# Optimization experiments

Hardware: AMD Instinct MI355X
Metric: run time of the kernel (lower is better)

Reference implementation:

```python
import jax, jax.numpy as jnp
import numpy as np
import math

GROUPS = 32
EPS = 1e-5
N_HEADS = 8  # channels=512 / num_head_channels=64


def group_norm(x, w, b):
    # x: [B, C, T]; GroupNorm over (channels-in-group, T)
    B, C, T = x.shape
    xg = x.reshape(B, GROUPS, C // GROUPS * T)
    mu = xg.mean(axis=-1, keepdims=True)
    var = xg.var(axis=-1, keepdims=True)
    xn = ((xg - mu) * jax.lax.rsqrt(var + EPS)).reshape(B, C, T)
    return xn * w[None, :, None] + b[None, :, None]


def setup_inputs() -> dict:
    key = jax.random.key(0)
    ks = jax.random.split(key, 7)
    C = 512
    return {
        "x": jax.random.normal(ks[0], (8, C, 32, 32), dtype=jnp.float32),
        "norm_w": jax.random.normal(ks[1], (C,), dtype=jnp.float32),
        "norm_b": jax.random.normal(ks[2], (C,), dtype=jnp.float32),
        "qkv_w": jax.random.normal(ks[3], (3 * C, C), dtype=jnp.float32) * 0.02,
        "qkv_b": jax.random.normal(ks[4], (3 * C,), dtype=jnp.float32) * 0.02,
        "proj_w": jax.random.normal(ks[5], (C, C), dtype=jnp.float32) * 0.02,
        "proj_b": jax.random.normal(ks[6], (C,), dtype=jnp.float32) * 0.02,
    }


def reference(x, norm_w, norm_b, qkv_w, qkv_b, proj_w, proj_b):
    b, c, H, W = x.shape
    T = H * W
    xf = x.reshape(b, c, T)
    xn = group_norm(xf, norm_w, norm_b)
    # 1x1 conv1d == channel matmul: [3C, C] x [B, C, T] -> [B, 3C, T]
    qkv = jnp.einsum('oc,bct->bot', qkv_w, xn) + qkv_b[None, :, None]
    ch = c // N_HEADS
    qkv = qkv.reshape(b * N_HEADS, 3 * ch, T)
    q, k, v = qkv[:, :ch], qkv[:, ch:2 * ch], qkv[:, 2 * ch:]
    scale = 1.0 / math.sqrt(math.sqrt(ch))
    # [BH, T, T] score matrix (explicit, as in the original)
    weight = jnp.einsum('bct,bcs->bts', q * scale, k * scale)
    weight = jax.nn.softmax(weight.astype(jnp.float32), axis=-1).astype(qkv.dtype)
    a = jnp.einsum('bts,bcs->bct', weight, v).reshape(b, c, T)
    hout = jnp.einsum('oc,bct->bot', proj_w, a) + proj_b[None, :, None]
    return (xf + hout).reshape(b, c, H, W)
```

## Files before the change

### kernel.cpp

```cpp
#include <hip/hip_runtime.h>
#include <math.h>

typedef float f32x4_t __attribute__((ext_vector_type(4)));
typedef short bf16x8_t __attribute__((ext_vector_type(8)));

#define B_   8
#define C_   512
#define T_   1024
#define NH_  8
#define CH_  64
#define EPSF 1e-5f

#define MFMA16(a, b, c) __builtin_amdgcn_mfma_f32_16x16x32_bf16((a), (b), (c), 0, 0, 0)

#define GLD16(gp, lp) __builtin_amdgcn_global_load_lds( \
    (const __attribute__((address_space(1))) unsigned int*)(gp), \
    (__attribute__((address_space(3))) unsigned int*)(lp), 16, 0, 0)

__device__ __forceinline__ unsigned short f2bf(float f) {
  union { float f; unsigned u; } v; v.f = f;
  unsigned r = v.u + 0x7FFFu + ((v.u >> 16) & 1u);
  return (unsigned short)(r >> 16);
}

__global__ __launch_bounds__(256) void prep_gn_kernel(
    const float* __restrict__ x, const float* __restrict__ w,
    const float* __restrict__ bvec, unsigned short* __restrict__ xnT,
    const float* __restrict__ qw_f, const float* __restrict__ pw_f,
    unsigned short* __restrict__ qw, unsigned short* __restrict__ pw)
{
  int tid = threadIdx.x;
  if (blockIdx.x >= 256) {
    int idx = (blockIdx.x - 256) * 256 + tid;
    const int N1 = 1536 * 512 / 4;
    const int N2 = 512 * 512 / 4;
    if (idx < N1) {
      float4 v = ((const float4*)qw_f)[idx];
      uint2 o;
      o.x = (unsigned)f2bf(v.x) | ((unsigned)f2bf(v.y) << 16);
      o.y = (unsigned)f2bf(v.z) | ((unsigned)f2bf(v.w) << 16);
      ((uint2*)qw)[idx] = o;
    } else if (idx < N1 + N2) {
      int j = idx - N1;
      float4 v = ((const float4*)pw_f)[j];
      uint2 o;
      o.x = (unsigned)f2bf(v.x) | ((unsigned)f2bf(v.y) << 16);
      o.y = (unsigned)f2bf(v.z) | ((unsigned)f2bf(v.w) << 16);
      ((uint2*)pw)[j] = o;
    }
    return;
  }

  int blk = blockIdx.x;
  int b = blk >> 5, g = blk & 31;
  const float* xp = x + ((size_t)(b * C_ + g * 16)) * T_;
  const int N = 16 * T_;

  float s = 0.f, s2 = 0.f;
  for (int i = tid * 4; i < N; i += 256 * 4) {
    float4 v = *(const float4*)(xp + i);
    s  += v.x + v.y + v.z + v.w;
    s2 += v.x * v.x + v.y * v.y + v.z * v.z + v.w * v.w;
  }
  for (int off = 32; off; off >>= 1) {
    s  += __shfl_down(s,  off, 64);
    s2 += __shfl_down(s2, off, 64);
  }
  __shared__ float rs_[4], r2_[4];
  __shared__ float mu_s, rsig_s;
  int wid = tid >> 6, lane = tid & 63;
  if (lane == 0) { rs_[wid] = s; r2_[wid] = s2; }
  __syncthreads();
  if (tid == 0) {
    float ts = rs_[0] + rs_[1] + rs_[2] + rs_[3];
    float t2 = r2_[0] + r2_[1] + r2_[2] + r2_[3];
    float mu = ts / (float)N;
    float var = t2 / (float)N - mu * mu;
    mu_s = mu;
    rsig_s = rsqrtf(var + EPSF);
  }
  __syncthreads();
  float mu = mu_s, rs = rsig_s;

  float wl[16], bl[16];
  for (int c = 0; c < 16; ++c) { wl[c] = w[g * 16 + c]; bl[c] = bvec[g * 16 + c]; }

  for (int t = tid; t < T_; t += 256) {
    unsigned short buf[16] __attribute__((aligned(16)));
    for (int c = 0; c < 16; ++c) {
      float val = xp[(size_t)c * T_ + t];
      buf[c] = f2bf((val - mu) * rs * wl[c] + bl[c]);
    }
    unsigned short* dst = xnT + ((size_t)b * T_ + t) * C_ + g * 16;
    *(uint4*)dst       = *(uint4*)buf;
    *(uint4*)(dst + 8) = *(uint4*)(buf + 8);
  }
}

__global__ __launch_bounds__(256) void gemm_qkv_kernel(
    const unsigned short* __restrict__ W, const unsigned short* __restrict__ xnT,
    const float* __restrict__ bias,
    unsigned short* __restrict__ q_t, unsigned short* __restrict__ k_t,
    unsigned short* __restrict__ v_c)
{
  int b = blockIdx.z;
  int m0 = blockIdx.y * 128, n0 = blockIdx.x * 128;
  int tid = threadIdx.x;
  int w = tid >> 6, lane = tid & 63, quad = lane >> 4, lr = lane & 15;
  int wm = w >> 1, wn = w & 1;

  __shared__ __align__(16) unsigned short Asl[2][128][32];
  __shared__ __align__(16) unsigned short Bsl[2][128][32];

  f32x4_t acc[4][4];
  for (int i = 0; i < 4; ++i)
    for (int j = 0; j < 4; ++j) acc[i][j] = (f32x4_t){0.f, 0.f, 0.f, 0.f};

  int ur = tid >> 2, uk = (tid & 3) * 8;
  const unsigned short* Ap = W + (size_t)(m0 + ur) * C_ + uk;
  const unsigned short* Bp = xnT + ((size_t)b * T_ + n0 + ur) * C_ + uk;

#define STAGE_QKV(buf, k0)                                        \
  do {                                                            \
    GLD16(Ap + (k0),            &Asl[buf][w * 16][0]);            \
    GLD16(Ap + 64 * C_ + (k0),  &Asl[buf][64 + w * 16][0]);       \
    GLD16(Bp + (k0),            &Bsl[buf][w * 16][0]);            \
    GLD16(Bp + 64 * C_ + (k0),  &Bsl[buf][64 + w * 16][0]);       \
  } while (0)

  STAGE_QKV(0, 0);
  __syncthreads();

  int cur = 0;
  for (int k0 = 0; k0 < C_; k0 += 32) {
    if (k0 + 32 < C_) STAGE_QKV(cur ^ 1, k0 + 32);
    bf16x8_t af[4], bfv[4];
    for (int i = 0; i < 4; ++i) af[i]  = *(bf16x8_t*)&Asl[cur][wm * 64 + i * 16 + lr][quad * 8];
    for (int j = 0; j < 4; ++j) bfv[j] = *(bf16x8_t*)&Bsl[cur][wn * 64 + j * 16 + lr][quad * 8];
    for (int i = 0; i < 4; ++i)
      for (int j = 0; j < 4; ++j)
        acc[i][j] = MFMA16(af[i], bfv[j], acc[i][j]);
    __syncthreads();
    cur ^= 1;
  }
#undef STAGE_QKV

  for (int i = 0; i < 4; ++i) {
    int ob = m0 + wm * 64 + i * 16 + quad * 4;
    int h = ob / 192, r0 = ob % 192;
    for (int j = 0; j < 4; ++j) {
      int t = n0 + wn * 64 + j * 16 + lr;
      if (r0 < 128) {
        unsigned short pk[4] __attribute__((aligned(8)));
      #pragma unroll
        for (int r = 0; r < 4; ++r) pk[r] = f2bf(acc[i][j][r] + bias[ob + r]);
        unsigned short* base = (r0 < 64) ? q_t : k_t;
        int chn = (r0 < 64) ? r0 : r0 - 64;
        *(uint2*)&base[((size_t)(b * NH_ + h) * T_ + t) * CH_ + chn] = *(uint2*)pk;
      } else {
      #pragma unroll
        for (int r = 0; r < 4; ++r) {
          float vv = acc[i][j][r] + bias[ob + r];
          v_c[((size_t)(b * NH_ + h) * CH_ + (r0 - 128 + r)) * T_ + t] = f2bf(vv);
        }
      }
    }
  }
}

__global__ __launch_bounds__(256) void attn_kernel(
    const unsigned short* __restrict__ q_t, const unsigned short* __restrict__ k_t,
    const unsigned short* __restrict__ v_c, unsigned short* __restrict__ a_t)
{
  int bh = blockIdx.x;
  int t0 = blockIdx.y * 128;
  int tid = threadIdx.x;
  int w = tid >> 6, lane = tid & 63, quad = lane >> 4, lr = lane & 15;

  __shared__ __align__(16) unsigned short q_s[128][72];
  __shared__ __align__(16) unsigned short p_s[128][72];
  __shared__ __align__(16) unsigned short k_s[64][72];
  __shared__ __align__(16) unsigned short v_s[64][72];

  int r0 = tid >> 3, c0 = (tid & 7) * 8;
#pragma unroll
  for (int cch = 0; cch < 4; ++cch)
    *(uint4*)&q_s[r0 + 32 * cch][c0] =
        *(const uint4*)&q_t[((size_t)bh * T_ + t0 + r0 + 32 * cch) * CH_ + c0];

  uint4 kr0 = *(const uint4*)&k_t[((size_t)bh * T_ + r0) * CH_ + c0];
  uint4 kr1 = *(const uint4*)&k_t[((size_t)bh * T_ + r0 + 32) * CH_ + c0];
  uint4 vr0 = *(const uint4*)&v_c[((size_t)bh * CH_ + r0) * T_ + c0];
  uint4 vr1 = *(const uint4*)&v_c[((size_t)bh * CH_ + r0 + 32) * T_ + c0];

  __syncthreads();
  bf16x8_t aq[2][2];
#pragma unroll
  for (int rb = 0; rb < 2; ++rb) {
    aq[rb][0] = *(bf16x8_t*)&q_s[w * 32 + rb * 16 + lr][quad * 8];
    aq[rb][1] = *(bf16x8_t*)&q_s[w * 32 + rb * 16 + lr][32 + quad * 8];
  }

  bf16x8_t ones8;
  {
    short ov = (lr == 0) ? (short)0x3F80 : (short)0;
    for (int e = 0; e < 8; ++e) ones8[e] = ov;
  }

  f32x4_t o_acc[2][4], o_l[2];
#pragma unroll
  for (int rb = 0; rb < 2; ++rb) {
    for (int j = 0; j < 4; ++j) o_acc[rb][j] = (f32x4_t){0.f, 0.f, 0.f, 0.f};
    o_l[rb] = (f32x4_t){0.f, 0.f, 0.f, 0.f};
  }

  const float SCL = 0.18033688f;
  const float MSH = 11.541560f;

  for (int s0 = 0; s0 < T_; s0 += 64) {
    __syncthreads();
    *(uint4*)&k_s[r0][c0]      = kr0;
    *(uint4*)&k_s[r0 + 32][c0] = kr1;
    *(uint4*)&v_s[r0][c0]      = vr0;
    *(uint4*)&v_s[r0 + 32][c0] = vr1;
    if (s0 + 64 < T_) {
      kr0 = *(const uint4*)&k_t[((size_t)bh * T_ + s0 + 64 + r0) * CH_ + c0];
      kr1 = *(const uint4*)&k_t[((size_t)bh * T_ + s0 + 96 + r0) * CH_ + c0];
      vr0 = *(const uint4*)&v_c[((size_t)bh * CH_ + r0) * T_ + s0 + 64 + c0];
      vr1 = *(const uint4*)&v_c[((size_t)bh * CH_ + r0 + 32) * T_ + s0 + 64 + c0];
    }
    __syncthreads();

    f32x4_t sc[2][4];
    __builtin_amdgcn_s_setprio(1);
#pragma unroll
    for (int j = 0; j < 4; ++j) {
      f32x4_t a0 = (f32x4_t){0.f, 0.f, 0.f, 0.f};
      f32x4_t a1 = (f32x4_t){0.f, 0.f, 0.f, 0.f};
#pragma unroll
      for (int kk = 0; kk < 2; ++kk) {
        bf16x8_t bk = *(bf16x8_t*)&k_s[j * 16 + lr][kk * 32 + quad * 8];
        a0 = MFMA16(aq[0][kk], bk, a0);
        a1 = MFMA16(aq[1][kk], bk, a1);
      }
      sc[0][j] = a0;
      sc[1][j] = a1;
    }
    __builtin_amdgcn_s_setprio(0);

#pragma unroll
    for (int rb = 0; rb < 2; ++rb)
#pragma unroll
      for (int j = 0; j < 4; ++j)
#pragma unroll
        for (int r = 0; r < 4; ++r) {
          float p = __builtin_amdgcn_exp2f(sc[rb][j][r] * SCL - MSH);
          union { float f; unsigned u; } cv; cv.f = p;
          p_s[w * 32 + rb * 16 + quad * 4 + r][j * 16 + lr] = (unsigned short)(cv.u >> 16);
        }
    bf16x8_t ap[2][2];
#pragma unroll
    for (int rb = 0; rb < 2; ++rb) {
      ap[rb][0] = *(bf16x8_t*)&p_s[w * 32 + rb * 16 + lr][quad * 8];
      ap[rb][1] = *(bf16x8_t*)&p_s[w * 32 + rb * 16 + lr][32 + quad * 8];
    }

    __builtin_amdgcn_s_setprio(1);
#pragma unroll
    for (int rb = 0; rb < 2; ++rb) {
      o_l[rb] = MFMA16(ap[rb][0], ones8, o_l[rb]);
      o_l[rb] = MFMA16(ap[rb][1], ones8, o_l[rb]);
    }
#pragma unroll
    for (int j = 0; j < 4; ++j)
#pragma unroll
      for (int kk = 0; kk < 2; ++kk) {
        bf16x8_t bv = *(bf16x8_t*)&v_s[j * 16 + lr][kk * 32 + quad * 8];
        o_acc[0][j] = MFMA16(ap[0][kk], bv, o_acc[0][j]);
        o_acc[1][j] = MFMA16(ap[1][kk], bv, o_acc[1][j]);
      }
    __builtin_amdgcn_s_setprio(0);
  }

#pragma unroll
  for (int rb = 0; rb < 2; ++rb) {
    float lv[4];
#pragma unroll
    for (int r = 0; r < 4; ++r) lv[r] = __shfl(o_l[rb][r], lane & 48, 64);
#pragma unroll
    for (int r = 0; r < 4; ++r) {
      float inv = 1.f / lv[r];
#pragma unroll
      for (int j = 0; j < 4; ++j)
        q_s[w * 32 + rb * 16 + quad * 4 + r][j * 16 + lr] = f2bf(o_acc[rb][j][r] * inv);
    }
  }
  __syncthreads();
#pragma unroll
  for (int cch = 0; cch < 4; ++cch)
    *(uint4*)&a_t[((size_t)bh * T_ + t0 + r0 + 32 * cch) * CH_ + c0] =
        *(uint4*)&q_s[r0 + 32 * cch][c0];
}

__global__ __launch_bounds__(256) void gemm_proj_kernel(
    const unsigned short* __restrict__ W, const unsigned short* __restrict__ a_t,
    const float* __restrict__ bias, const float* __restrict__ xres,
    float* __restrict__ out)
{
  int b = blockIdx.z;
  int m0 = blockIdx.y * 128, n0 = blockIdx.x * 128;
  int tid = threadIdx.x;
  int w = tid >> 6, lane = tid & 63, quad = lane >> 4, lr = lane & 15;
  int wm = w >> 1, wn = w & 1;

  __shared__ __align__(16) unsigned short Asl[2][128][32];
  __shared__ __align__(16) unsigned short Bsl[2][128][32];

  f32x4_t acc[4][4];
  for (int i = 0; i < 4; ++i)
    for (int j = 0; j < 4; ++j) acc[i][j] = (f32x4_t){0.f, 0.f, 0.f, 0.f};

  int ur = tid >> 2, uk = (tid & 3) * 8;
  const unsigned short* Ap = W + (size_t)(m0 + ur) * C_ + uk;

#define STAGE_PROJ(buf, k0)                                                   \
  do {                                                                        \
    const unsigned short* Bp = a_t +                                          \
        ((size_t)(b * NH_ + ((k0) >> 6)) * T_ + n0 + ur) * CH_ + ((k0) & 63) + uk; \
    GLD16(Ap + (k0),           &Asl[buf][w * 16][0]);                         \
    GLD16(Ap + 64 * C_ + (k0), &Asl[buf][64 + w * 16][0]);                    \
    GLD16(Bp,                  &Bsl[buf][w * 16][0]);                         \
    GLD16(Bp + 64 * CH_,       &Bsl[buf][64 + w * 16][0]);                    \
  } while (0)

  STAGE_PROJ(0, 0);
  __syncthreads();

  int cur = 0;
  for (int k0 = 0; k0 < C_; k0 += 32) {
    if (k0 + 32 < C_) STAGE_PROJ(cur ^ 1, k0 + 32);
    bf16x8_t af[4], bfv[4];
    for (int i = 0; i < 4; ++i) af[i]  = *(bf16x8_t*)&Asl[cur][wm * 64 + i * 16 + lr][quad * 8];
    for (int j = 0; j < 4; ++j) bfv[j] = *(bf16x8_t*)&Bsl[cur][wn * 64 + j * 16 + lr][quad * 8];
    for (int i = 0; i < 4; ++i)
      for (int j = 0; j < 4; ++j)
        acc[i][j] = MFMA16(af[i], bfv[j], acc[i][j]);
    __syncthreads();
    cur ^= 1;
  }
#undef STAGE_PROJ

  for (int i = 0; i < 4; ++i) {
    int ob = m0 + wm * 64 + i * 16 + quad * 4;
    for (int j = 0; j < 4; ++j) {
      int t = n0 + wn * 64 + j * 16 + lr;
    #pragma unroll
      for (int r = 0; r < 4; ++r) {
        size_t idx = ((size_t)(b * C_ + ob + r)) * T_ + t;
        out[idx] = acc[i][j][r] + bias[ob + r] + xres[idx];
      }
    }
  }
}

extern "C" void kernel_launch(void* const* d_in, const int* in_sizes, int n_in,
                              void* d_out, int out_size, void* d_ws, size_t ws_size,
                              hipStream_t stream)
{
  const float* x      = (const float*)d_in[0];
  const float* norm_w = (const float*)d_in[1];
  const float* norm_b = (const float*)d_in[2];
  const float* qkv_w  = (const float*)d_in[3];
  const float* qkv_b  = (const float*)d_in[4];
  const float* proj_w = (const float*)d_in[5];
  const float* proj_b = (const float*)d_in[6];
  float* out = (float*)d_out;

  char* ws = (char*)d_ws;
  unsigned short* qw  = (unsigned short*)ws;
  unsigned short* pw  = (unsigned short*)(ws + 1572864);
  unsigned short* xnT = (unsigned short*)(ws + 2097152);
  unsigned short* q_t = (unsigned short*)(ws + 10485760);
  unsigned short* k_t = (unsigned short*)(ws + 18874368);
  unsigned short* v_c = (unsigned short*)(ws + 27262976);
  unsigned short* a_t = (unsigned short*)(ws + 35651584);

  prep_gn_kernel<<<dim3(256 + 1024), dim3(256), 0, stream>>>(
      x, norm_w, norm_b, xnT, qkv_w, proj_w, qw, pw);

  gemm_qkv_kernel<<<dim3(T_ / 128, 1536 / 128, B_), dim3(256), 0, stream>>>(
      qw, xnT, qkv_b, q_t, k_t, v_c);

  attn_kernel<<<dim3(B_ * NH_, T_ / 128), dim3(256), 0, stream>>>(q_t, k_t, v_c, a_t);

  gemm_proj_kernel<<<dim3(T_ / 128, C_ / 128, B_), dim3(256), 0, stream>>>(
      pw, a_t, proj_b, x, out);
}
```

Measured before the change: 164.1 us.

## Transpose score MFMA, vectorize P stores, compute row sums in registers

```diff
diff --git a/kernel.cpp b/kernel.cpp
--- a/kernel.cpp
+++ b/kernel.cpp
@@ -29,6 +29,10 @@
     const float* __restrict__ qw_f, const float* __restrict__ pw_f,
     unsigned short* __restrict__ qw, unsigned short* __restrict__ pw)
 {
+  __shared__ __align__(16) float xs[16 * 1024];
+  __shared__ float rs_[4], r2_[4];
+  __shared__ float mu_s, rsig_s;
+
   int tid = threadIdx.x;
   if (blockIdx.x >= 256) {
     int idx = (blockIdx.x - 256) * 256 + tid;
@@ -59,6 +63,7 @@
   float s = 0.f, s2 = 0.f;
   for (int i = tid * 4; i < N; i += 256 * 4) {
     float4 v = *(const float4*)(xp + i);
+    *(float4*)&xs[i] = v;
     s  += v.x + v.y + v.z + v.w;
     s2 += v.x * v.x + v.y * v.y + v.z * v.z + v.w * v.w;
   }
@@ -66,8 +71,6 @@
     s  += __shfl_down(s,  off, 64);
     s2 += __shfl_down(s2, off, 64);
   }
-  __shared__ float rs_[4], r2_[4];
-  __shared__ float mu_s, rsig_s;
   int wid = tid >> 6, lane = tid & 63;
   if (lane == 0) { rs_[wid] = s; r2_[wid] = s2; }
   __syncthreads();
@@ -88,7 +91,7 @@
   for (int t = tid; t < T_; t += 256) {
     unsigned short buf[16] __attribute__((aligned(16)));
     for (int c = 0; c < 16; ++c) {
-      float val = xp[(size_t)c * T_ + t];
+      float val = xs[c * T_ + t];
       buf[c] = f2bf((val - mu) * rs * wl[c] + bl[c]);
     }
     unsigned short* dst = xnT + ((size_t)b * T_ + t) * C_ + g * 16;
@@ -194,25 +197,18 @@
   uint4 vr1 = *(const uint4*)&v_c[((size_t)bh * CH_ + r0 + 32) * T_ + c0];
 
   __syncthreads();
-  bf16x8_t aq[2][2];
+  bf16x8_t bq[2][2];
 #pragma unroll
   for (int rb = 0; rb < 2; ++rb) {
-    aq[rb][0] = *(bf16x8_t*)&q_s[w * 32 + rb * 16 + lr][quad * 8];
-    aq[rb][1] = *(bf16x8_t*)&q_s[w * 32 + rb * 16 + lr][32 + quad * 8];
-  }
-
-  bf16x8_t ones8;
-  {
-    short ov = (lr == 0) ? (short)0x3F80 : (short)0;
-    for (int e = 0; e < 8; ++e) ones8[e] = ov;
-  }
-
-  f32x4_t o_acc[2][4], o_l[2];
-#pragma unroll
-  for (int rb = 0; rb < 2; ++rb) {
+    bq[rb][0] = *(bf16x8_t*)&q_s[w * 32 + rb * 16 + lr][quad * 8];
+    bq[rb][1] = *(bf16x8_t*)&q_s[w * 32 + rb * 16 + lr][32 + quad * 8];
+  }
+
+  f32x4_t o_acc[2][4];
+#pragma unroll
+  for (int rb = 0; rb < 2; ++rb)
     for (int j = 0; j < 4; ++j) o_acc[rb][j] = (f32x4_t){0.f, 0.f, 0.f, 0.f};
-    o_l[rb] = (f32x4_t){0.f, 0.f, 0.f, 0.f};
-  }
+  float l_sum[2] = {0.f, 0.f};
 
   const float SCL = 0.18033688f;
   const float MSH = 11.541560f;
@@ -231,33 +227,47 @@
     }
     __syncthreads();
 
-    f32x4_t sc[2][4];
+    f32x4_t sc[4][2];
     __builtin_amdgcn_s_setprio(1);
 #pragma unroll
     for (int j = 0; j < 4; ++j) {
+      bf16x8_t ak0 = *(bf16x8_t*)&k_s[j * 16 + lr][quad * 8];
+      bf16x8_t ak1 = *(bf16x8_t*)&k_s[j * 16 + lr][32 + quad * 8];
       f32x4_t a0 = (f32x4_t){0.f, 0.f, 0.f, 0.f};
       f32x4_t a1 = (f32x4_t){0.f, 0.f, 0.f, 0.f};
-#pragma unroll
-      for (int kk = 0; kk < 2; ++kk) {
-        bf16x8_t bk = *(bf16x8_t*)&k_s[j * 16 + lr][kk * 32 + quad * 8];
-        a0 = MFMA16(aq[0][kk], bk, a0);
-        a1 = MFMA16(aq[1][kk], bk, a1);
+      a0 = MFMA16(ak0, bq[0][0], a0);
+      a0 = MFMA16(ak1, bq[0][1], a0);
+      a1 = MFMA16(ak0, bq[1][0], a1);
+      a1 = MFMA16(ak1, bq[1][1], a1);
+      sc[j][0] = a0;
+      sc[j][1] = a1;
+    }
+    __builtin_amdgcn_s_setprio(0);
+
+#pragma unroll
+    for (int rb = 0; rb < 2; ++rb) {
+      float rsum = 0.f;
+#pragma unroll
+      for (int j = 0; j < 4; ++j) {
+        unsigned u[4];
+#pragma unroll
+        for (int r = 0; r < 4; ++r) {
+          union { float f; unsigned v; } cv;
+          cv.f = __builtin_amdgcn_exp2f(sc[j][rb][r] * SCL - MSH);
+          u[r] = cv.v & 0xFFFF0000u;
+          union { unsigned v; float f; } rf; rf.v = u[r];
+          rsum += rf.f;
+        }
+        uint2 pk;
+        pk.x = (u[0] >> 16) | u[1];
+        pk.y = (u[2] >> 16) | u[3];
+        *(uint2*)&p_s[w * 32 + rb * 16 + lr][j * 16 + quad * 4] = pk;
       }
-      sc[0][j] = a0;
-      sc[1][j] = a1;
-    }
-    __builtin_amdgcn_s_setprio(0);
-
-#pragma unroll
-    for (int rb = 0; rb < 2; ++rb)
-#pragma unroll
-      for (int j = 0; j < 4; ++j)
-#pragma unroll
-        for (int r = 0; r < 4; ++r) {
-          float p = __builtin_amdgcn_exp2f(sc[rb][j][r] * SCL - MSH);
-          union { float f; unsigned u; } cv; cv.f = p;
-          p_s[w * 32 + rb * 16 + quad * 4 + r][j * 16 + lr] = (unsigned short)(cv.u >> 16);
-        }
+      rsum += __shfl_xor(rsum, 16, 64);
+      rsum += __shfl_xor(rsum, 32, 64);
+      l_sum[rb] += rsum;
+    }
+
     bf16x8_t ap[2][2];
 #pragma unroll
     for (int rb = 0; rb < 2; ++rb) {
@@ -266,11 +276,6 @@
     }
 
     __builtin_amdgcn_s_setprio(1);
-#pragma unroll
-    for (int rb = 0; rb < 2; ++rb) {
-      o_l[rb] = MFMA16(ap[rb][0], ones8, o_l[rb]);
-      o_l[rb] = MFMA16(ap[rb][1], ones8, o_l[rb]);
-    }
 #pragma unroll
     for (int j = 0; j < 4; ++j)
 #pragma unroll
@@ -284,12 +289,10 @@
 
 #pragma unroll
   for (int rb = 0; rb < 2; ++rb) {
-    float lv[4];
-#pragma unroll
-    for (int r = 0; r < 4; ++r) lv[r] = __shfl(o_l[rb][r], lane & 48, 64);
 #pragma unroll
     for (int r = 0; r < 4; ++r) {
-      float inv = 1.f / lv[r];
+      float lv = __shfl(l_sum[rb], quad * 4 + r, 64);
+      float inv = 1.f / lv;
 #pragma unroll
       for (int j = 0; j < 4; ++j)
         q_s[w * 32 + rb * 16 + quad * 4 + r][j * 16 + lr] = f2bf(o_acc[rb][j][r] * inv);
```

New measurement: 162.6 us. Within noise of the previous version (-0.9%).
